# Optimization experiments

Measured on AMD Instinct MI355X. Metric: run time of the kernel, lower is better.

The kernel has to match this reference:

```python
import jax, jax.numpy as jnp
import numpy as np

# ---- static config (from init_kwargs) ----
UP = 2
DOWN = 2
NEG_SLOPE = 0.2
MARGIN = 10
FLRELU_SCALE = np.float32(2.0 ** 0.5)  # fused_leaky_relu default scale
# p = K - factor = 12 - 2 = 10; padding=True branch
UP_PAD = ((10 + 1) // 2 + UP - 1, 10 // 2)      # (6, 5)
DOWN_PAD = ((10 + 1) // 2, 10 // 2)             # (5, 5)

# 12-tap hann-windowed-sinc lowpass (sum normalized to 1), as in alias-free GAN
_FILT = np.array([0.0, 0.00398, -0.01884, -0.05155, 0.12443, 0.44197,
                  0.44197, 0.12443, -0.05155, -0.01884, 0.00398, 0.0],
                 dtype=np.float32)
_FILT = _FILT / _FILT.sum()


def _fir1d(x, k, up, down, pad0, pad1, axis):
    """upfirdn along one spatial axis of NCHW x with 1D kernel k.

    Matches upfirdn2d_native: zero-stuff by `up` (including up-1 trailing
    zeros, folded into right padding), pad, correlate with flipped kernel
    (= FIR convolution), stride-`down` subsample.
    """
    N, C, H, W = x.shape
    xr = x.reshape(N * C, 1, H, W)
    K = k.shape[0]
    kf = k[::-1].astype(x.dtype)  # flip -> true convolution, as in native op
    if axis == 3:  # width
        w = kf.reshape(1, 1, 1, K)
        lhs_dil = (1, up)
        strides = (1, down)
        padding = ((0, 0), (pad0, pad1 + up - 1))
    else:          # height
        w = kf.reshape(1, 1, K, 1)
        lhs_dil = (up, 1)
        strides = (down, 1)
        padding = ((pad0, pad1 + up - 1), (0, 0))
    y = jax.lax.conv_general_dilated(
        xr, w, window_strides=strides, padding=padding,
        lhs_dilation=lhs_dil, dimension_numbers=('NCHW', 'OIHW', 'NCHW'))
    return y.reshape(N, C, y.shape[2], y.shape[3])


def _sep_upfirdn(x, k, up, down, pad):
    # module applies the separable 1D filter along width first, then height,
    # with the same (pad0, pad1) on each axis
    x = _fir1d(x, k, up, down, pad[0], pad[1], axis=3)
    x = _fir1d(x, k, up, down, pad[0], pad[1], axis=2)
    return x


def setup_inputs() -> dict:
    key = jax.random.key(0)
    k_in = jax.random.fold_in(key, 0)
    return {
        'input': jax.random.normal(k_in, (8, 512, 64, 64), dtype=jnp.float32),
        'bias': jnp.zeros((512,), dtype=jnp.float32),
        'up_filter': jnp.asarray(_FILT),
        'down_filter': jnp.asarray(_FILT),
    }


def reference(input, bias, up_filter, down_filter):
    out = input + bias[None, :, None, None]
    # 1D upsample filter is pre-scaled by the upsample factor at init
    upf = up_filter * UP
    out = _sep_upfirdn(out, upf, UP, 1, UP_PAD)          # 64 -> 128
    out = jax.nn.leaky_relu(out, NEG_SLOPE) * FLRELU_SCALE
    out = _sep_upfirdn(out, down_filter, 1, DOWN, DOWN_PAD)  # 128 -> 64
    m = (MARGIN * UP - MARGIN * DOWN) // 2
    if m > 0:
        out = out[:, :, m:-m, m:-m]
    return out
```

## Files before the change

### kernel.cpp

```cpp
#include <hip/hip_runtime.h>

#define TPB 512
#define H 64
#define W 64

#define NT1 72
#define T1_STRIDE 132
#define T1_FLOATS (NT1 * T1_STRIDE)
#define T2_STRIDE 140
#define T2_OFF 4
#define LDS_FLOATS T1_FLOATS

typedef float v2f __attribute__((ext_vector_type(2)));

__global__ __launch_bounds__(TPB, 6)
void afa_fused(const float* __restrict__ in, const float* __restrict__ bias,
               const float* __restrict__ upf, const float* __restrict__ dnf,
               float* __restrict__ out)
{
    __shared__ __align__(16) float lds[LDS_FLOATS];
    float* const s_t1 = lds;
    float* const s_t2 = lds;

    const int tid = threadIdx.x;
    const int plane = blockIdx.x;

    float gA[5], gB[5], fhx[5], fhy[5], fd[11];
#pragma unroll
    for (int k = 0; k < 5; ++k) {
        gA[k]  = 2.0f * upf[9 - 2*k];
        gB[k]  = 2.0f * upf[10 - 2*k];
        fhx[k] = 1.41421356237309515f * dnf[2*k + 1];
        fhy[k] = 1.41421356237309515f * dnf[2*k + 2];
    }
#pragma unroll
    for (int k = 1; k <= 10; ++k) fd[k] = dnf[k];
    const float bv = bias[plane & 511];

    if (tid < 264) {
        *(float2*)(s_t1 + 2 * tid) = make_float2(0.f, 0.f);
        *(float2*)(s_t1 + 68 * T1_STRIDE + 2 * tid) = make_float2(0.f, 0.f);
    }

    {
        const int r  = tid >> 3;
        const int cb = tid & 7;
        const float4* p4 = (const float4*)(in + (size_t)plane * (H * W) + r * W);
        float4 q0 = p4[cb == 0 ? 0 : 2 * cb - 1];
        const float4 q1 = p4[2 * cb];
        const float4 q2 = p4[2 * cb + 1];
        float4 q3 = p4[cb == 7 ? 15 : 2 * cb + 2];
        if (cb == 0) q0 = make_float4(0.f, 0.f, 0.f, 0.f);
        if (cb == 7) q3 = make_float4(0.f, 0.f, 0.f, 0.f);
        float xr[12] = {q0.z, q0.w, q1.x, q1.y, q1.z, q1.w,
                        q2.x, q2.y, q2.z, q2.w, q3.x, q3.y};
        float o[16];
#pragma unroll
        for (int q = 0; q < 8; ++q) {
            float e = xr[q] * gA[0];
            float d = xr[q] * gB[0];
#pragma unroll
            for (int k = 1; k < 5; ++k) {
                e = fmaf(xr[q + k], gA[k], e);
                d = fmaf(xr[q + k], gB[k], d);
            }
            o[2*q] = e; o[2*q+1] = d;
        }
        float* dst = s_t1 + (r + 4) * T1_STRIDE + 16 * cb;
#pragma unroll
        for (int k = 0; k < 4; ++k)
            *(float4*)(dst + 4 * k) = make_float4(o[4*k], o[4*k+1], o[4*k+2], o[4*k+3]);
    }
    __syncthreads();

    const int c = tid & 63;
    const int q = tid >> 6;
    float accx[8] = {0.f,0.f,0.f,0.f,0.f,0.f,0.f,0.f};
    float accy[8] = {0.f,0.f,0.f,0.f,0.f,0.f,0.f,0.f};
    {
        v2f cc[16];
#pragma unroll
        for (int t = 0; t < 16; ++t)
            cc[t] = *(const v2f*)(s_t1 + (8 * q + t) * T1_STRIDE + 2 * c);
        const bool mlo = (q == 0);
        const bool mhi = (q == 7);
#pragma unroll
        for (int t = 0; t < 12; ++t) {
            float tax = fmaf(cc[t].x, gA[0], bv);
            float tay = fmaf(cc[t].y, gA[0], bv);
            float tbx = fmaf(cc[t].x, gB[0], bv);
            float tby = fmaf(cc[t].y, gB[0], bv);
#pragma unroll
            for (int k = 1; k < 5; ++k) {
                tax = fmaf(cc[t + k].x, gA[k], tax);
                tay = fmaf(cc[t + k].y, gA[k], tay);
                tbx = fmaf(cc[t + k].x, gB[k], tbx);
                tby = fmaf(cc[t + k].y, gB[k], tby);
            }
            if (mlo && t < 2)   { tax = 0.f; tay = 0.f; tbx = 0.f; tby = 0.f; }
            if (mhi && t >= 10) { tax = 0.f; tay = 0.f; tbx = 0.f; tby = 0.f; }
            const float rax = fmaxf(tax, 0.2f * tax);
            const float ray = fmaxf(tay, 0.2f * tay);
            const float rbx = fmaxf(tbx, 0.2f * tbx);
            const float rby = fmaxf(tby, 0.2f * tby);
#pragma unroll
            for (int p = 0; p < 8; ++p) {
                if (p <= t && t <= p + 4) {
                    const int m = 4 - (t - p);
                    accx[p] = fmaf(rax, fhy[m], fmaf(rbx, fhx[m], accx[p]));
                    accy[p] = fmaf(ray, fhy[m], fmaf(rby, fhx[m], accy[p]));
                }
            }
        }
    }
    __syncthreads();

#pragma unroll
    for (int p = 0; p < 8; ++p)
        *(v2f*)(s_t2 + (8 * q + p) * T2_STRIDE + T2_OFF + 2 * c) = (v2f){accx[p], accy[p]};
    {
        const int rw = tid >> 3, cz = tid & 7;
        s_t2[rw * T2_STRIDE + (cz < 4 ? cz : 128 + cz)] = 0.f;
    }
    __syncthreads();

#pragma unroll
    for (int s_ = 0; s_ < 2; ++s_) {
        const int u = tid + 512 * s_;
        const int oy = u >> 4, oxb = u & 15;
        const float* base = s_t2 + oy * T2_STRIDE + 8 * oxb;
        float wv[16];
#pragma unroll
        for (int t = 0; t < 4; ++t) {
            const float4 v = *(const float4*)(base + 4 * t);
            wv[4*t] = v.x; wv[4*t+1] = v.y; wv[4*t+2] = v.z; wv[4*t+3] = v.w;
        }
        float o2[4];
#pragma unroll
        for (int p = 0; p < 4; ++p) {
            float a2 = 0.f;
#pragma unroll
            for (int k = 0; k < 10; ++k)
                a2 = fmaf(wv[2*p + k], fd[10 - k], a2);
            o2[p] = a2;
        }
        float* po = out + (size_t)plane * (H * W) + oy * W + 4 * oxb;
        *(float4*)po = make_float4(o2[0], o2[1], o2[2], o2[3]);
    }
}

extern "C" void kernel_launch(void* const* d_in, const int* in_sizes, int n_in,
                              void* d_out, int out_size, void* d_ws, size_t ws_size,
                              hipStream_t stream) {
    const float* in  = (const float*)d_in[0];
    const float* bv  = (const float*)d_in[1];
    const float* upf = (const float*)d_in[2];
    const float* dnf = (const float*)d_in[3];
    float* out = (float*)d_out;
    const int planes = 8 * 512;
    afa_fused<<<planes, TPB, 0, stream>>>(in, bv, upf, dnf, out);
}
```

Before: 42.19 us.

## Process 8 planes per block with software-pipelined loads and bf16 intermediate

Each block now loops over 8 planes. It prefetches the next plane's input into registers and overlaps the previous plane's horizontal downsample with the current plane's first pass. The second intermediate buffer is stored as packed bf16 in separate LDS, which shrinks LDS traffic and allows a separate buffer so fewer barriers are needed. The trade-offs are reduced precision in the intermediate, a grid of only 512 blocks (about 2 per CU), and lower occupancy per launch bound.

```diff
diff --git a/kernel.cpp b/kernel.cpp
--- a/kernel.cpp
+++ b/kernel.cpp
@@ -1,29 +1,30 @@
 #include <hip/hip_runtime.h>
 
 #define TPB 512
-#define H 64
-#define W 64
-
-#define NT1 72
-#define T1_STRIDE 132
-#define T1_FLOATS (NT1 * T1_STRIDE)
-#define T2_STRIDE 140
-#define T2_OFF 4
-#define LDS_FLOATS T1_FLOATS
+#define PPB 8
+#define T1S 132
+#define T2S 72
 
 typedef float v2f __attribute__((ext_vector_type(2)));
 
-__global__ __launch_bounds__(TPB, 6)
+__device__ __forceinline__ unsigned int bf2(float a, float b) {
+    unsigned int ua = __float_as_uint(a), ub = __float_as_uint(b);
+    ua = (ua + 0x7FFFu + ((ua >> 16) & 1u)) >> 16;
+    ub = (ub + 0x7FFFu + ((ub >> 16) & 1u)) & 0xFFFF0000u;
+    return ua | ub;
+}
+
+__global__ __launch_bounds__(TPB, 4)
 void afa_fused(const float* __restrict__ in, const float* __restrict__ bias,
                const float* __restrict__ upf, const float* __restrict__ dnf,
                float* __restrict__ out)
 {
-    __shared__ __align__(16) float lds[LDS_FLOATS];
-    float* const s_t1 = lds;
-    float* const s_t2 = lds;
+    __shared__ __align__(16) float        s_t1[72 * T1S];
+    __shared__ __align__(16) unsigned int s_t2[64 * T2S];
 
     const int tid = threadIdx.x;
-    const int plane = blockIdx.x;
+    const int ri = tid >> 3, cb = tid & 7;
+    const int c  = tid & 63, q = tid >> 6;
 
     float gA[5], gB[5], fhx[5], fhy[5], fd[11];
 #pragma unroll
@@ -35,118 +36,136 @@
     }
 #pragma unroll
     for (int k = 1; k <= 10; ++k) fd[k] = dnf[k];
-    const float bv = bias[plane & 511];
 
     if (tid < 264) {
         *(float2*)(s_t1 + 2 * tid) = make_float2(0.f, 0.f);
-        *(float2*)(s_t1 + 68 * T1_STRIDE + 2 * tid) = make_float2(0.f, 0.f);
+        *(float2*)(s_t1 + 68 * T1S + 2 * tid) = make_float2(0.f, 0.f);
+    }
+    if (tid < 256) {
+        const int rw = tid >> 2, k = tid & 3;
+        s_t2[rw * T2S + ((k < 2) ? k : 64 + k)] = 0u;
     }
 
-    {
-        const int r  = tid >> 3;
-        const int cb = tid & 7;
-        const float4* p4 = (const float4*)(in + (size_t)plane * (H * W) + r * W);
-        float4 q0 = p4[cb == 0 ? 0 : 2 * cb - 1];
-        const float4 q1 = p4[2 * cb];
-        const float4 q2 = p4[2 * cb + 1];
-        float4 q3 = p4[cb == 7 ? 15 : 2 * cb + 2];
-        if (cb == 0) q0 = make_float4(0.f, 0.f, 0.f, 0.f);
-        if (cb == 7) q3 = make_float4(0.f, 0.f, 0.f, 0.f);
-        float xr[12] = {q0.z, q0.w, q1.x, q1.y, q1.z, q1.w,
-                        q2.x, q2.y, q2.z, q2.w, q3.x, q3.y};
-        float o[16];
+    const int plane0 = blockIdx.x * PPB;
+
+    const float4* px = (const float4*)(in + (size_t)plane0 * 4096 + ri * 64);
+    float4 x0 = px[cb == 0 ? 0 : 2 * cb - 1];
+    float4 x1 = px[2 * cb];
+    float4 x2 = px[2 * cb + 1];
+    float4 x3 = px[cb == 7 ? 15 : 2 * cb + 2];
+
+    auto wdown = [&](float* op) {
 #pragma unroll
-        for (int q = 0; q < 8; ++q) {
-            float e = xr[q] * gA[0];
-            float d = xr[q] * gB[0];
+        for (int s_ = 0; s_ < 2; ++s_) {
+            const int u = tid + TPB * s_;
+            const int oy = u >> 4, oxb = u & 15;
+            const unsigned int* b = s_t2 + oy * T2S + 4 * oxb;
+            const uint4 wA = *(const uint4*)(b);
+            const uint4 wB = *(const uint4*)(b + 4);
+            float wv[16];
+            {
+                const unsigned int ws[8] = {wA.x, wA.y, wA.z, wA.w, wB.x, wB.y, wB.z, wB.w};
 #pragma unroll
-            for (int k = 1; k < 5; ++k) {
-                e = fmaf(xr[q + k], gA[k], e);
-                d = fmaf(xr[q + k], gB[k], d);
-            }
-            o[2*q] = e; o[2*q+1] = d;
-        }
-        float* dst = s_t1 + (r + 4) * T1_STRIDE + 16 * cb;
-#pragma unroll
-        for (int k = 0; k < 4; ++k)
-            *(float4*)(dst + 4 * k) = make_float4(o[4*k], o[4*k+1], o[4*k+2], o[4*k+3]);
-    }
-    __syncthreads();
-
-    const int c = tid & 63;
-    const int q = tid >> 6;
-    float accx[8] = {0.f,0.f,0.f,0.f,0.f,0.f,0.f,0.f};
-    float accy[8] = {0.f,0.f,0.f,0.f,0.f,0.f,0.f,0.f};
-    {
-        v2f cc[16];
-#pragma unroll
-        for (int t = 0; t < 16; ++t)
-            cc[t] = *(const v2f*)(s_t1 + (8 * q + t) * T1_STRIDE + 2 * c);
-        const bool mlo = (q == 0);
-        const bool mhi = (q == 7);
-#pragma unroll
-        for (int t = 0; t < 12; ++t) {
-            float tax = fmaf(cc[t].x, gA[0], bv);
-            float tay = fmaf(cc[t].y, gA[0], bv);
-            float tbx = fmaf(cc[t].x, gB[0], bv);
-            float tby = fmaf(cc[t].y, gB[0], bv);
-#pragma unroll
-            for (int k = 1; k < 5; ++k) {
-                tax = fmaf(cc[t + k].x, gA[k], tax);
-                tay = fmaf(cc[t + k].y, gA[k], tay);
-                tbx = fmaf(cc[t + k].x, gB[k], tbx);
-                tby = fmaf(cc[t + k].y, gB[k], tby);
-            }
-            if (mlo && t < 2)   { tax = 0.f; tay = 0.f; tbx = 0.f; tby = 0.f; }
-            if (mhi && t >= 10) { tax = 0.f; tay = 0.f; tbx = 0.f; tby = 0.f; }
-            const float rax = fmaxf(tax, 0.2f * tax);
-            const float ray = fmaxf(tay, 0.2f * tay);
-            const float rbx = fmaxf(tbx, 0.2f * tbx);
-            const float rby = fmaxf(tby, 0.2f * tby);
-#pragma unroll
-            for (int p = 0; p < 8; ++p) {
-                if (p <= t && t <= p + 4) {
-                    const int m = 4 - (t - p);
-                    accx[p] = fmaf(rax, fhy[m], fmaf(rbx, fhx[m], accx[p]));
-                    accy[p] = fmaf(ray, fhy[m], fmaf(rby, fhx[m], accy[p]));
+                for (int k = 0; k < 8; ++k) {
+                    wv[2*k]   = __uint_as_float(ws[k] << 16);
+                    wv[2*k+1] = __uint_as_float(ws[k] & 0xFFFF0000u);
                 }
             }
+            float o2[4];
+#pragma unroll
+            for (int p2 = 0; p2 < 4; ++p2) {
+                float a2 = 0.f;
+#pragma unroll
+                for (int k = 0; k < 10; ++k)
+                    a2 = fmaf(wv[2*p2 + k], fd[10 - k], a2);
+                o2[p2] = a2;
+            }
+            *(float4*)(op + oy * 64 + 4 * oxb) = make_float4(o2[0], o2[1], o2[2], o2[3]);
         }
+    };
+
+    for (int p = 0; p < PPB; ++p) {
+        const int plane = plane0 + p;
+        const float bv = bias[plane & 511];
+
+        if (p > 0)
+            wdown(out + (size_t)(plane - 1) * 4096);
+
+        {
+            const float4 z4 = make_float4(0.f, 0.f, 0.f, 0.f);
+            const float4 q0 = (cb == 0) ? z4 : x0;
+            const float4 q3 = (cb == 7) ? z4 : x3;
+            const float xr[12] = {q0.z, q0.w, x1.x, x1.y, x1.z, x1.w,
+                                  x2.x, x2.y, x2.z, x2.w, q3.x, q3.y};
+            float* dst = s_t1 + (ri + 4) * T1S + 16 * cb;
+#pragma unroll
+            for (int h = 0; h < 4; ++h) {
+                const int qq = 2 * h;
+                float o0 = xr[qq] * gA[0],     o1 = xr[qq] * gB[0];
+                float o2_ = xr[qq + 1] * gA[0], o3 = xr[qq + 1] * gB[0];
+#pragma unroll
+                for (int k = 1; k < 5; ++k) {
+                    o0  = fmaf(xr[qq + k],     gA[k], o0);
+                    o1  = fmaf(xr[qq + k],     gB[k], o1);
+                    o2_ = fmaf(xr[qq + 1 + k], gA[k], o2_);
+                    o3  = fmaf(xr[qq + 1 + k], gB[k], o3);
+                }
+                *(float4*)(dst + 4 * h) = make_float4(o0, o1, o2_, o3);
+            }
+        }
+        if (p + 1 < PPB) {
+            const float4* pn = (const float4*)(in + (size_t)(plane + 1) * 4096 + ri * 64);
+            x0 = pn[cb == 0 ? 0 : 2 * cb - 1];
+            x1 = pn[2 * cb];
+            x2 = pn[2 * cb + 1];
+            x3 = pn[cb == 7 ? 15 : 2 * cb + 2];
+        }
+        __syncthreads();
+
+        {
+            v2f cc[16];
+#pragma unroll
+            for (int t = 0; t < 16; ++t)
+                cc[t] = *(const v2f*)(s_t1 + (8 * q + t) * T1S + 2 * c);
+            float accx[8] = {0.f,0.f,0.f,0.f,0.f,0.f,0.f,0.f};
+            float accy[8] = {0.f,0.f,0.f,0.f,0.f,0.f,0.f,0.f};
+            const bool mlo = (q == 0), mhi = (q == 7);
+#pragma unroll
+            for (int t = 0; t < 12; ++t) {
+                float tax = fmaf(cc[t].x, gA[0], bv);
+                float tay = fmaf(cc[t].y, gA[0], bv);
+                float tbx = fmaf(cc[t].x, gB[0], bv);
+                float tby = fmaf(cc[t].y, gB[0], bv);
+#pragma unroll
+                for (int k = 1; k < 5; ++k) {
+                    tax = fmaf(cc[t + k].x, gA[k], tax);
+                    tay = fmaf(cc[t + k].y, gA[k], tay);
+                    tbx = fmaf(cc[t + k].x, gB[k], tbx);
+                    tby = fmaf(cc[t + k].y, gB[k], tby);
+                }
+                if (mlo && t < 2)   { tax = 0.f; tay = 0.f; tbx = 0.f; tby = 0.f; }
+                if (mhi && t >= 10) { tax = 0.f; tay = 0.f; tbx = 0.f; tby = 0.f; }
+                const float rax = fmaxf(tax, 0.2f * tax);
+                const float ray = fmaxf(tay, 0.2f * tay);
+                const float rbx = fmaxf(tbx, 0.2f * tbx);
+                const float rby = fmaxf(tby, 0.2f * tby);
+#pragma unroll
+                for (int pp = 0; pp < 8; ++pp) {
+                    if (pp <= t && t <= pp + 4) {
+                        const int m = 4 - (t - pp);
+                        accx[pp] = fmaf(rax, fhy[m], fmaf(rbx, fhx[m], accx[pp]));
+                        accy[pp] = fmaf(ray, fhy[m], fmaf(rby, fhx[m], accy[pp]));
+                    }
+                }
+            }
+#pragma unroll
+            for (int pp = 0; pp < 8; ++pp)
+                s_t2[(8 * q + pp) * T2S + 2 + c] = bf2(accx[pp], accy[pp]);
+        }
+        __syncthreads();
     }
-    __syncthreads();
 
-#pragma unroll
-    for (int p = 0; p < 8; ++p)
-        *(v2f*)(s_t2 + (8 * q + p) * T2_STRIDE + T2_OFF + 2 * c) = (v2f){accx[p], accy[p]};
-    {
-        const int rw = tid >> 3, cz = tid & 7;
-        s_t2[rw * T2_STRIDE + (cz < 4 ? cz : 128 + cz)] = 0.f;
-    }
-    __syncthreads();
-
-#pragma unroll
-    for (int s_ = 0; s_ < 2; ++s_) {
-        const int u = tid + 512 * s_;
-        const int oy = u >> 4, oxb = u & 15;
-        const float* base = s_t2 + oy * T2_STRIDE + 8 * oxb;
-        float wv[16];
-#pragma unroll
-        for (int t = 0; t < 4; ++t) {
-            const float4 v = *(const float4*)(base + 4 * t);
-            wv[4*t] = v.x; wv[4*t+1] = v.y; wv[4*t+2] = v.z; wv[4*t+3] = v.w;
-        }
-        float o2[4];
-#pragma unroll
-        for (int p = 0; p < 4; ++p) {
-            float a2 = 0.f;
-#pragma unroll
-            for (int k = 0; k < 10; ++k)
-                a2 = fmaf(wv[2*p + k], fd[10 - k], a2);
-            o2[p] = a2;
-        }
-        float* po = out + (size_t)plane * (H * W) + oy * W + 4 * oxb;
-        *(float4*)po = make_float4(o2[0], o2[1], o2[2], o2[3]);
-    }
+    wdown(out + (size_t)(plane0 + PPB - 1) * 4096);
 }
 
 extern "C" void kernel_launch(void* const* d_in, const int* in_sizes, int n_in,
@@ -157,6 +176,5 @@
     const float* upf = (const float*)d_in[2];
     const float* dnf = (const float*)d_in[3];
     float* out = (float*)d_out;
-    const int planes = 8 * 512;
-    afa_fused<<<planes, TPB, 0, stream>>>(in, bv, upf, dnf, out);
+    afa_fused<<<4096 / PPB, TPB, 0, stream>>>(in, bv, upf, dnf, out);
 }
```

Result: slower. 50.99 us (+20.9%).

## Store LDS intermediates as packed bf16 and split into two LDS buffers

Applied to the files above, without the earlier changes.

Intermediate tiles held in shared memory are now stored as packed bf16 pairs (v_cvt_pk_bf16_f32) instead of fp32. This halves LDS footprint and traffic. The t1 and t2 buffers are separated, which removes one __syncthreads between the vertical pass and the t2 write, and launch bounds drop from 6 to 4 waves. The cost is reduced precision in the intermediates, which may exceed the tolerance, plus some unpack ALU work.

```diff
diff --git a/kernel.cpp b/kernel.cpp
--- a/kernel.cpp
+++ b/kernel.cpp
@@ -4,23 +4,25 @@
 #define H 64
 #define W 64
 
-#define NT1 72
-#define T1_STRIDE 132
-#define T1_FLOATS (NT1 * T1_STRIDE)
-#define T2_STRIDE 140
-#define T2_OFF 4
-#define LDS_FLOATS T1_FLOATS
+#define P1 68
+#define P2 68
+#define LDS_BYTES ((72 * P1 + 64 * P2) * 4)
 
-typedef float v2f __attribute__((ext_vector_type(2)));
+__device__ __forceinline__ unsigned int pkbf(float lo, float hi) {
+    unsigned int d;
+    asm("v_cvt_pk_bf16_f32 %0, %1, %2" : "=v"(d) : "v"(lo), "v"(hi));
+    return d;
+}
+__device__ __forceinline__ float ulo(unsigned int u) { return __uint_as_float(u << 16); }
+__device__ __forceinline__ float uhi(unsigned int u) { return __uint_as_float(u & 0xFFFF0000u); }
 
-__global__ __launch_bounds__(TPB, 6)
+__global__ __launch_bounds__(TPB, 4)
 void afa_fused(const float* __restrict__ in, const float* __restrict__ bias,
                const float* __restrict__ upf, const float* __restrict__ dnf,
                float* __restrict__ out)
 {
-    __shared__ __align__(16) float lds[LDS_FLOATS];
-    float* const s_t1 = lds;
-    float* const s_t2 = lds;
+    __shared__ __align__(16) unsigned int s_t1u[72 * P1];
+    __shared__ __align__(16) unsigned int s_t2u[64 * P2];
 
     const int tid = threadIdx.x;
     const int plane = blockIdx.x;
@@ -37,23 +39,25 @@
     for (int k = 1; k <= 10; ++k) fd[k] = dnf[k];
     const float bv = bias[plane & 511];
 
-    if (tid < 264) {
-        *(float2*)(s_t1 + 2 * tid) = make_float2(0.f, 0.f);
-        *(float2*)(s_t1 + 68 * T1_STRIDE + 2 * tid) = make_float2(0.f, 0.f);
+    if (tid < 256) {
+        const int r = tid >> 6, cc0 = tid & 63;
+        s_t1u[r * P1 + cc0] = 0u;
+        s_t1u[(68 + r) * P1 + cc0] = 0u;
+        const int rw = tid >> 2, k = tid & 3;
+        s_t2u[rw * P2 + ((k < 2) ? k : 64 + k)] = 0u;
     }
 
     {
-        const int r  = tid >> 3;
-        const int cb = tid & 7;
-        const float4* p4 = (const float4*)(in + (size_t)plane * (H * W) + r * W);
+        const int ri = tid >> 3, cb = tid & 7;
+        const float4* p4 = (const float4*)(in + (size_t)plane * (H * W) + ri * W);
         float4 q0 = p4[cb == 0 ? 0 : 2 * cb - 1];
         const float4 q1 = p4[2 * cb];
         const float4 q2 = p4[2 * cb + 1];
         float4 q3 = p4[cb == 7 ? 15 : 2 * cb + 2];
         if (cb == 0) q0 = make_float4(0.f, 0.f, 0.f, 0.f);
         if (cb == 7) q3 = make_float4(0.f, 0.f, 0.f, 0.f);
-        float xr[12] = {q0.z, q0.w, q1.x, q1.y, q1.z, q1.w,
-                        q2.x, q2.y, q2.z, q2.w, q3.x, q3.y};
+        const float xr[12] = {q0.z, q0.w, q1.x, q1.y, q1.z, q1.w,
+                              q2.x, q2.y, q2.z, q2.w, q3.x, q3.y};
         float o[16];
 #pragma unroll
         for (int q = 0; q < 8; ++q) {
@@ -66,36 +70,38 @@
             }
             o[2*q] = e; o[2*q+1] = d;
         }
-        float* dst = s_t1 + (r + 4) * T1_STRIDE + 16 * cb;
-#pragma unroll
-        for (int k = 0; k < 4; ++k)
-            *(float4*)(dst + 4 * k) = make_float4(o[4*k], o[4*k+1], o[4*k+2], o[4*k+3]);
+        uint4* dst = (uint4*)(s_t1u + (ri + 4) * P1 + 8 * cb);
+        dst[0] = make_uint4(pkbf(o[0], o[1]),  pkbf(o[2], o[3]),
+                            pkbf(o[4], o[5]),  pkbf(o[6], o[7]));
+        dst[1] = make_uint4(pkbf(o[8], o[9]),  pkbf(o[10], o[11]),
+                            pkbf(o[12], o[13]), pkbf(o[14], o[15]));
     }
     __syncthreads();
 
-    const int c = tid & 63;
-    const int q = tid >> 6;
-    float accx[8] = {0.f,0.f,0.f,0.f,0.f,0.f,0.f,0.f};
-    float accy[8] = {0.f,0.f,0.f,0.f,0.f,0.f,0.f,0.f};
     {
-        v2f cc[16];
+        const int c = tid & 63;
+        const int q = tid >> 6;
+        float ccx[16], ccy[16];
 #pragma unroll
-        for (int t = 0; t < 16; ++t)
-            cc[t] = *(const v2f*)(s_t1 + (8 * q + t) * T1_STRIDE + 2 * c);
-        const bool mlo = (q == 0);
-        const bool mhi = (q == 7);
+        for (int t = 0; t < 16; ++t) {
+            const unsigned int u = s_t1u[(8 * q + t) * P1 + c];
+            ccx[t] = ulo(u); ccy[t] = uhi(u);
+        }
+        float accx[8] = {0.f,0.f,0.f,0.f,0.f,0.f,0.f,0.f};
+        float accy[8] = {0.f,0.f,0.f,0.f,0.f,0.f,0.f,0.f};
+        const bool mlo = (q == 0), mhi = (q == 7);
 #pragma unroll
         for (int t = 0; t < 12; ++t) {
-            float tax = fmaf(cc[t].x, gA[0], bv);
-            float tay = fmaf(cc[t].y, gA[0], bv);
-            float tbx = fmaf(cc[t].x, gB[0], bv);
-            float tby = fmaf(cc[t].y, gB[0], bv);
+            float tax = fmaf(ccx[t], gA[0], bv);
+            float tay = fmaf(ccy[t], gA[0], bv);
+            float tbx = fmaf(ccx[t], gB[0], bv);
+            float tby = fmaf(ccy[t], gB[0], bv);
 #pragma unroll
             for (int k = 1; k < 5; ++k) {
-                tax = fmaf(cc[t + k].x, gA[k], tax);
-                tay = fmaf(cc[t + k].y, gA[k], tay);
-                tbx = fmaf(cc[t + k].x, gB[k], tbx);
-                tby = fmaf(cc[t + k].y, gB[k], tby);
+                tax = fmaf(ccx[t + k], gA[k], tax);
+                tay = fmaf(ccy[t + k], gA[k], tay);
+                tbx = fmaf(ccx[t + k], gB[k], tbx);
+                tby = fmaf(ccy[t + k], gB[k], tby);
             }
             if (mlo && t < 2)   { tax = 0.f; tay = 0.f; tbx = 0.f; tby = 0.f; }
             if (mhi && t >= 10) { tax = 0.f; tay = 0.f; tbx = 0.f; tby = 0.f; }
@@ -104,45 +110,39 @@
             const float rbx = fmaxf(tbx, 0.2f * tbx);
             const float rby = fmaxf(tby, 0.2f * tby);
 #pragma unroll
-            for (int p = 0; p < 8; ++p) {
-                if (p <= t && t <= p + 4) {
-                    const int m = 4 - (t - p);
-                    accx[p] = fmaf(rax, fhy[m], fmaf(rbx, fhx[m], accx[p]));
-                    accy[p] = fmaf(ray, fhy[m], fmaf(rby, fhx[m], accy[p]));
+            for (int pp = 0; pp < 8; ++pp) {
+                if (pp <= t && t <= pp + 4) {
+                    const int m = 4 - (t - pp);
+                    accx[pp] = fmaf(rax, fhy[m], fmaf(rbx, fhx[m], accx[pp]));
+                    accy[pp] = fmaf(ray, fhy[m], fmaf(rby, fhx[m], accy[pp]));
                 }
             }
         }
-    }
-    __syncthreads();
-
 #pragma unroll
-    for (int p = 0; p < 8; ++p)
-        *(v2f*)(s_t2 + (8 * q + p) * T2_STRIDE + T2_OFF + 2 * c) = (v2f){accx[p], accy[p]};
-    {
-        const int rw = tid >> 3, cz = tid & 7;
-        s_t2[rw * T2_STRIDE + (cz < 4 ? cz : 128 + cz)] = 0.f;
+        for (int pp = 0; pp < 8; ++pp)
+            s_t2u[(8 * q + pp) * P2 + 2 + c] = pkbf(accx[pp], accy[pp]);
     }
     __syncthreads();
 
 #pragma unroll
     for (int s_ = 0; s_ < 2; ++s_) {
-        const int u = tid + 512 * s_;
+        const int u = tid + TPB * s_;
         const int oy = u >> 4, oxb = u & 15;
-        const float* base = s_t2 + oy * T2_STRIDE + 8 * oxb;
+        const unsigned int* b = s_t2u + oy * P2 + 4 * oxb;
+        const uint4 wA = *(const uint4*)(b);
+        const uint4 wB = *(const uint4*)(b + 4);
+        const unsigned int ws[8] = {wA.x, wA.y, wA.z, wA.w, wB.x, wB.y, wB.z, wB.w};
         float wv[16];
 #pragma unroll
-        for (int t = 0; t < 4; ++t) {
-            const float4 v = *(const float4*)(base + 4 * t);
-            wv[4*t] = v.x; wv[4*t+1] = v.y; wv[4*t+2] = v.z; wv[4*t+3] = v.w;
-        }
+        for (int k = 0; k < 8; ++k) { wv[2*k] = ulo(ws[k]); wv[2*k+1] = uhi(ws[k]); }
         float o2[4];
 #pragma unroll
-        for (int p = 0; p < 4; ++p) {
+        for (int p2 = 0; p2 < 4; ++p2) {
             float a2 = 0.f;
 #pragma unroll
             for (int k = 0; k < 10; ++k)
-                a2 = fmaf(wv[2*p + k], fd[10 - k], a2);
-            o2[p] = a2;
+                a2 = fmaf(wv[2*p2 + k], fd[10 - k], a2);
+            o2[p2] = a2;
         }
         float* po = out + (size_t)plane * (H * W) + oy * W + 4 * oxb;
         *(float4*)po = make_float4(o2[0], o2[1], o2[2], o2[3]);
@@ -157,6 +157,5 @@
     const float* upf = (const float*)d_in[2];
     const float* dnf = (const float*)d_in[3];
     float* out = (float*)d_out;
-    const int planes = 8 * 512;
-    afa_fused<<<planes, TPB, 0, stream>>>(in, bv, upf, dnf, out);
+    afa_fused<<<8 * 512, TPB, 0, stream>>>(in, bv, upf, dnf, out);
 }
```

Result: slower. 47.59 us (+12.8%).
